# Kernel optimization log

Measured on AMD Instinct MI355X. Metric: run time of the kernel, lower is better.

The kernel has to match this reference:

```python
import jax, jax.numpy as jnp
import numpy as np

NUM_HEADS = 16
PREFIX_LEN = 256


def setup_inputs() -> dict:
    key = jax.random.key(0)
    k1, k2, k3, k4 = jax.random.split(key, 4)
    bs, seq_len, dim = 2, 2048, 1024
    x = jax.random.normal(k1, (bs, seq_len, dim), dtype=jnp.float32)
    # torch Linear weights: (out_features, in_features)
    qkv_w = jax.random.normal(k2, (3 * dim, dim), dtype=jnp.float32) * (dim ** -0.5)
    proj_w = jax.random.normal(k3, (dim, dim), dtype=jnp.float32) * (dim ** -0.5)
    proj_b = jax.random.normal(k4, (dim,), dtype=jnp.float32) * 0.01
    # prefix tokens (visible to everyone): first PREFIX_LEN positions
    prefix_mask = (jnp.arange(seq_len)[None, :] < PREFIX_LEN) & jnp.ones((bs, 1), bool)
    return {"x": x, "qkv_w": qkv_w, "proj_w": proj_w, "proj_b": proj_b,
            "prefix_mask": prefix_mask, "num_patches": 2048}


def reference(x, qkv_w, proj_w, proj_b, prefix_mask, num_patches):
    bs, seq_len, dim = x.shape
    h, hd = NUM_HEADS, dim // NUM_HEADS

    # fused QKV projection (no bias)
    qkv = x @ qkv_w.T                                  # (bs, S, 3*dim)
    q, k, v = jnp.split(qkv, 3, axis=-1)
    q = q.reshape(bs, seq_len, h, hd).transpose(0, 2, 1, 3)  # (bs, h, S, hd)
    k = k.reshape(bs, seq_len, h, hd).transpose(0, 2, 1, 3)
    v = v.reshape(bs, seq_len, h, hd).transpose(0, 2, 1, 3)

    # prefix-causal mask: causal tril OR prefix columns, sliced to (S, S)
    tril = jnp.tril(jnp.ones((num_patches, num_patches), dtype=bool))[:seq_len, :seq_len]
    mask = jnp.logical_or(tril[None, :, :], prefix_mask[:, None, :])  # (bs, S, S)

    scores = jnp.einsum('bhqd,bhkd->bhqk', q, k) / jnp.sqrt(jnp.float32(hd))
    scores = jnp.where(mask[:, None, :, :], scores, -jnp.inf)
    attn = jax.nn.softmax(scores, axis=-1)
    out = jnp.einsum('bhqk,bhkd->bhqd', attn, v)       # (bs, h, S, hd)
    out = out.transpose(0, 2, 1, 3).reshape(bs, seq_len, dim)
    return out @ proj_w.T + proj_b
```

## Files before the change

kernel.cpp:

```cpp
#include <hip/hip_runtime.h>
#include <cstdint>

typedef __attribute__((ext_vector_type(8))) _Float16 half8;
typedef __attribute__((ext_vector_type(4))) _Float16 half4;
typedef __attribute__((ext_vector_type(2))) __fp16 fp16x2;
typedef __attribute__((ext_vector_type(4))) float f32x4;

union H8 { half8 v; unsigned u[4]; };
union H2U { fp16x2 h; unsigned u; };

__device__ __forceinline__ void gld_lds16(const void* g, void* l) {
  __builtin_amdgcn_global_load_lds(
      (const __attribute__((address_space(1))) unsigned int*)g,
      (__attribute__((address_space(3))) unsigned int*)l, 16, 0, 0);
}

__global__ __launch_bounds__(256) void cast3_kernel(
    const float* __restrict__ x, const float* __restrict__ w1,
    const float* __restrict__ w2, _Float16* __restrict__ out) {
  int i = blockIdx.x * 256 + threadIdx.x;
  const float* src;
  int off;
  if (i < 1048576)      { src = x;  off = i; }
  else if (i < 1835008) { src = w1; off = i - 1048576; }
  else                  { src = w2; off = i - 1835008; }
  float4 v = ((const float4*)src)[off];
  half4 h;
  h[0] = (_Float16)v.x; h[1] = (_Float16)v.y;
  h[2] = (_Float16)v.z; h[3] = (_Float16)v.w;
  ((half4*)out)[i] = h;
}

template <int EPI>
__global__ __launch_bounds__(256) void gemm_bt(
    const _Float16* __restrict__ A, const _Float16* __restrict__ B, int K,
    _Float16* __restrict__ Qb, _Float16* __restrict__ Kb, _Float16* __restrict__ VbT,
    float* __restrict__ Out, const float* __restrict__ Bias) {
  __shared__ _Float16 Asm[2][128 * 32];
  __shared__ _Float16 Bsm[2][128 * 32];
  const int tid = threadIdx.x;
  const int wave = tid >> 6, lane = tid & 63;
  const int l16 = lane & 15, lg = lane >> 4;
  const int m0 = blockIdx.y * 128, n0 = blockIdx.x * 128;
  const int wr = wave >> 1, wc = wave & 1;
  f32x4 acc[4][4] = {};

  const int d0 = tid, d1 = tid + 256;
  const int row0 = d0 >> 2, cc0 = (d0 & 3) ^ ((row0 >> 1) & 3);
  const int row1 = d1 >> 2, cc1 = (d1 & 3) ^ ((row1 >> 1) & 3);
  const int sread = ((lg ^ ((l16 >> 1) & 3))) * 16;

  auto STAGE = [&](int buf, int k0) {
    gld_lds16(A + (size_t)(m0 + row0) * K + k0 + cc0 * 8, (char*)Asm[buf] + d0 * 16);
    gld_lds16(A + (size_t)(m0 + row1) * K + k0 + cc1 * 8, (char*)Asm[buf] + d1 * 16);
    gld_lds16(B + (size_t)(n0 + row0) * K + k0 + cc0 * 8, (char*)Bsm[buf] + d0 * 16);
    gld_lds16(B + (size_t)(n0 + row1) * K + k0 + cc1 * 8, (char*)Bsm[buf] + d1 * 16);
  };

  STAGE(0, 0);
  int cur = 0;
  for (int k0 = 0; k0 < K; k0 += 32) {
    __syncthreads();
    if (k0 + 32 < K) STAGE(cur ^ 1, k0 + 32);
    const char* Ac = (const char*)Asm[cur];
    const char* Bc = (const char*)Bsm[cur];
    half8 af[4], bf[4];
#pragma unroll
    for (int f = 0; f < 4; f++) {
      af[f] = *(const half8*)(Ac + (wr * 64 + f * 16 + l16) * 64 + sread);
      bf[f] = *(const half8*)(Bc + (wc * 64 + f * 16 + l16) * 64 + sread);
    }
#pragma unroll
    for (int i = 0; i < 4; i++)
#pragma unroll
      for (int j = 0; j < 4; j++)
        acc[i][j] = __builtin_amdgcn_mfma_f32_16x16x32_f16(af[i], bf[j], acc[i][j], 0, 0, 0);
    cur ^= 1;
  }

  if (EPI == 0) {
#pragma unroll
    for (int i = 0; i < 4; i++) {
      int mbase = m0 + wr * 64 + i * 16 + lg * 4;
      int b = mbase >> 11, s = mbase & 2047;
#pragma unroll
      for (int j = 0; j < 4; j++) {
        int n = n0 + wc * 64 + j * 16 + l16;
        int part = n >> 10, f = n & 1023;
        int h = f >> 6, d = f & 63;
        if (part == 2) {
          int x = s & 31;
          int sp = (s & ~31) | (((x >> 2) & 3) << 3) | (((x >> 4) & 1) << 2);
          half4 v;
          v[0] = (_Float16)acc[i][j][0]; v[1] = (_Float16)acc[i][j][1];
          v[2] = (_Float16)acc[i][j][2]; v[3] = (_Float16)acc[i][j][3];
          *(half4*)(VbT + (((size_t)b * 16 + h) * 64 + d) * 2048 + sp) = v;
        } else {
          _Float16* dst = (part == 0) ? Qb : Kb;
          float scale = (part == 0) ? 0.18033688f : 1.0f;
#pragma unroll
          for (int r = 0; r < 4; r++)
            dst[(((size_t)b * 16 + h) * 2048 + (s + r)) * 64 + d] =
                (_Float16)(acc[i][j][r] * scale);
        }
      }
    }
  } else {
#pragma unroll
    for (int i = 0; i < 4; i++) {
      int mbase = m0 + wr * 64 + i * 16 + lg * 4;
#pragma unroll
      for (int j = 0; j < 4; j++) {
        int n = n0 + wc * 64 + j * 16 + l16;
        float bias = Bias[n];
#pragma unroll
        for (int r = 0; r < 4; r++) {
          int m = mbase + r;
          Out[(size_t)m * 1024 + n] = acc[i][j][r] + bias;
        }
      }
    }
  }
}

__global__ __launch_bounds__(256) void attn_kernel(
    const _Float16* __restrict__ Qb, const _Float16* __restrict__ Kb,
    const _Float16* __restrict__ VbT, _Float16* __restrict__ AO) {
  __shared__ _Float16 Ks[2][64 * 64];
  __shared__ _Float16 Vt[2][64 * 64];
  const int bh = blockIdx.x;
  const int q0 = (31 - blockIdx.y) * 64;
  const int tid = threadIdx.x, wave = tid >> 6, lane = tid & 63;
  const int l16 = lane & 15, lg = lane >> 4;
  const int qw = q0 + wave * 16;
  const size_t bhbase = (size_t)bh * 2048 * 64;
  const _Float16* Kbb = Kb + bhbase;
  const _Float16* Vbb = VbT + bhbase;

  const int c0 = tid, c1 = tid + 256;
  const int kofs0 = ((c0 >> 3) * 64) + (((c0 & 7) ^ ((c0 >> 3) & 7)) * 8);
  const int kofs1 = ((c1 >> 3) * 64) + (((c1 & 7) ^ ((c1 >> 3) & 7)) * 8);
  const int vofs0 = ((c0 >> 3) * 2048) + (((c0 & 7) ^ ((c0 >> 3) & 7)) * 8);
  const int vofs1 = ((c1 >> 3) * 2048) + (((c1 & 7) ^ ((c1 >> 3) & 7)) * 8);

  half8 qf[2];
#pragma unroll
  for (int kc = 0; kc < 2; kc++)
    qf[kc] = *(const half8*)(Qb + bhbase + (size_t)(qw + l16) * 64 + kc * 32 + lg * 8);

  f32x4 oacc[4] = {};
  float lrun = 0.f;
  const int kend = (q0 + 64 > 256) ? (q0 + 64) : 256;

  const int xv = (l16 & 7) << 4;
  const int rb0 = l16 * 128 + ((lg * 16) ^ xv);
  const int rb1 = l16 * 128 + ((64 + lg * 16) ^ xv);

  auto STAGE = [&](int buf, int j0) {
    gld_lds16(Kbb + j0 * 64 + kofs0, (char*)Ks[buf] + c0 * 16);
    gld_lds16(Kbb + j0 * 64 + kofs1, (char*)Ks[buf] + c1 * 16);
    gld_lds16(Vbb + j0 + vofs0, (char*)Vt[buf] + c0 * 16);
    gld_lds16(Vbb + j0 + vofs1, (char*)Vt[buf] + c1 * 16);
  };

  STAGE(0, 0);
  int cur = 0;
  for (int j0 = 0; j0 < kend; j0 += 64) {
    __syncthreads();
    if (j0 + 64 < kend) STAGE(cur ^ 1, j0 + 64);
    const char* Kc = (const char*)Ks[cur];
    const char* Vc = (const char*)Vt[cur];

    f32x4 sf[4] = {};
    __builtin_amdgcn_s_setprio(1);
#pragma unroll
    for (int kc = 0; kc < 2; kc++) {
      const int rb = kc ? rb1 : rb0;
#pragma unroll
      for (int jb = 0; jb < 4; jb++) {
        half8 kf = *(const half8*)(Kc + jb * 2048 + rb);
        sf[jb] = __builtin_amdgcn_mfma_f32_16x16x32_f16(kf, qf[kc], sf[jb], 0, 0, 0);
      }
    }
    __builtin_amdgcn_s_setprio(0);

    if (j0 + 63 >= 256 && j0 + 63 > qw) {
      const int stok = qw + l16;
#pragma unroll
      for (int jb = 0; jb < 4; jb++)
#pragma unroll
        for (int r = 0; r < 4; r++) {
          int j = j0 + jb * 16 + lg * 4 + r;
          if (j > stok && j >= 256) sf[jb][r] = -1e30f;
        }
    }

    float p[16];
#pragma unroll
    for (int jb = 0; jb < 4; jb++)
#pragma unroll
      for (int r = 0; r < 4; r++)
        p[jb * 4 + r] = exp2f(sf[jb][r]);

    float s0 = (p[0] + p[1]) + (p[2] + p[3]);
    float s1 = (p[4] + p[5]) + (p[6] + p[7]);
    float s2 = (p[8] + p[9]) + (p[10] + p[11]);
    float s3 = (p[12] + p[13]) + (p[14] + p[15]);
    lrun += (s0 + s1) + (s2 + s3);

    H8 pf[2];
#pragma unroll
    for (int kc = 0; kc < 2; kc++) {
      H2U t0, t1, t2, t3;
      t0.h = __builtin_amdgcn_cvt_pkrtz(p[kc * 8 + 0], p[kc * 8 + 1]);
      t1.h = __builtin_amdgcn_cvt_pkrtz(p[kc * 8 + 2], p[kc * 8 + 3]);
      t2.h = __builtin_amdgcn_cvt_pkrtz(p[kc * 8 + 4], p[kc * 8 + 5]);
      t3.h = __builtin_amdgcn_cvt_pkrtz(p[kc * 8 + 6], p[kc * 8 + 7]);
      pf[kc].u[0] = t0.u; pf[kc].u[1] = t1.u;
      pf[kc].u[2] = t2.u; pf[kc].u[3] = t3.u;
    }

    __builtin_amdgcn_s_setprio(1);
#pragma unroll
    for (int kc = 0; kc < 2; kc++) {
      const int rb = kc ? rb1 : rb0;
#pragma unroll
      for (int db = 0; db < 4; db++) {
        half8 vf = *(const half8*)(Vc + db * 2048 + rb);
        oacc[db] = __builtin_amdgcn_mfma_f32_16x16x32_f16(vf, pf[kc].v, oacc[db], 0, 0, 0);
      }
    }
    __builtin_amdgcn_s_setprio(0);
    cur ^= 1;
  }

  lrun += __shfl_xor(lrun, 16);
  lrun += __shfl_xor(lrun, 32);

  const int b = bh >> 4, h = bh & 15;
  float inv = 1.0f / lrun;
  int q = qw + l16;
#pragma unroll
  for (int db = 0; db < 4; db++) {
    half4 o;
    o[0] = (_Float16)(oacc[db][0] * inv);
    o[1] = (_Float16)(oacc[db][1] * inv);
    o[2] = (_Float16)(oacc[db][2] * inv);
    o[3] = (_Float16)(oacc[db][3] * inv);
    *(half4*)(AO + ((size_t)b * 2048 + q) * 1024 + h * 64 + db * 16 + lg * 4) = o;
  }
}

extern "C" void kernel_launch(void* const* d_in, const int* in_sizes, int n_in,
                              void* d_out, int out_size, void* d_ws, size_t ws_size,
                              hipStream_t stream) {
  const float* x      = (const float*)d_in[0];
  const float* qkv_w  = (const float*)d_in[1];
  const float* proj_w = (const float*)d_in[2];
  const float* proj_b = (const float*)d_in[3];
  float* out = (float*)d_out;

  char* ws = (char*)d_ws;
  _Float16* Xh  = (_Float16*)(ws);
  _Float16* Wq  = (_Float16*)(ws + ((size_t)8 << 20));
  _Float16* Wp  = (_Float16*)(ws + ((size_t)14 << 20));
  _Float16* Qb  = (_Float16*)(ws + ((size_t)16 << 20));
  _Float16* Kb  = (_Float16*)(ws + ((size_t)24 << 20));
  _Float16* VbT = (_Float16*)(ws + ((size_t)32 << 20));
  _Float16* AO  = (_Float16*)(ws + ((size_t)40 << 20));

  cast3_kernel<<<8192, 256, 0, stream>>>(x, qkv_w, proj_w, Xh);

  gemm_bt<0><<<dim3(24, 32), 256, 0, stream>>>(Xh, Wq, 1024, Qb, Kb, VbT, nullptr, nullptr);
  attn_kernel<<<dim3(32, 32), 256, 0, stream>>>(Qb, Kb, VbT, AO);
  gemm_bt<1><<<dim3(8, 32), 256, 0, stream>>>(AO, Wp, 1024, nullptr, nullptr, nullptr, out, proj_b);
}
```

Baseline: 182.1 us.

## Halve attention query tile and load V fragments directly from global memory

The attention kernel now uses 32-query blocks with 2 waves (128 threads) instead of 64-query blocks with 4 waves, doubling the grid to 32x64. This gives finer causal load balance and more blocks for occupancy. V is no longer staged through LDS; each wave reads its V^T fragments straight from global memory into registers, which halves LDS use. The cost is that K tiles are reused by fewer waves, and the uncached V reads raise global/L2 traffic and latency that is no longer double-buffered.

```diff
diff --git a/kernel.cpp b/kernel.cpp
--- a/kernel.cpp
+++ b/kernel.cpp
@@ -123,44 +123,46 @@
   }
 }
 
-__global__ __launch_bounds__(256) void attn_kernel(
+__global__ __launch_bounds__(128) void attn_kernel(
     const _Float16* __restrict__ Qb, const _Float16* __restrict__ Kb,
     const _Float16* __restrict__ VbT, _Float16* __restrict__ AO) {
   __shared__ _Float16 Ks[2][64 * 64];
-  __shared__ _Float16 Vt[2][64 * 64];
   const int bh = blockIdx.x;
-  const int q0 = (31 - blockIdx.y) * 64;
+  const int q0 = (63 - blockIdx.y) * 32;
   const int tid = threadIdx.x, wave = tid >> 6, lane = tid & 63;
   const int l16 = lane & 15, lg = lane >> 4;
   const int qw = q0 + wave * 16;
   const size_t bhbase = (size_t)bh * 2048 * 64;
   const _Float16* Kbb = Kb + bhbase;
-  const _Float16* Vbb = VbT + bhbase;
-
-  const int c0 = tid, c1 = tid + 256;
-  const int kofs0 = ((c0 >> 3) * 64) + (((c0 & 7) ^ ((c0 >> 3) & 7)) * 8);
-  const int kofs1 = ((c1 >> 3) * 64) + (((c1 & 7) ^ ((c1 >> 3) & 7)) * 8);
-  const int vofs0 = ((c0 >> 3) * 2048) + (((c0 & 7) ^ ((c0 >> 3) & 7)) * 8);
-  const int vofs1 = ((c1 >> 3) * 2048) + (((c1 & 7) ^ ((c1 >> 3) & 7)) * 8);
+
+  int kofs[4], cdst[4];
+#pragma unroll
+  for (int i = 0; i < 4; i++) {
+    int c = tid + i * 128;
+    cdst[i] = c;
+    kofs[i] = ((c >> 3) * 64) + (((c & 7) ^ ((c >> 3) & 7)) * 8);
+  }
 
   half8 qf[2];
 #pragma unroll
   for (int kc = 0; kc < 2; kc++)
     qf[kc] = *(const half8*)(Qb + bhbase + (size_t)(qw + l16) * 64 + kc * 32 + lg * 8);
 
+  const _Float16* Vl = VbT + bhbase + (size_t)l16 * 2048 + lg * 8;
+
   f32x4 oacc[4] = {};
   float lrun = 0.f;
-  const int kend = (q0 + 64 > 256) ? (q0 + 64) : 256;
+  int kend = (q0 + 32 + 63) & ~63;
+  if (kend < 256) kend = 256;
 
   const int xv = (l16 & 7) << 4;
   const int rb0 = l16 * 128 + ((lg * 16) ^ xv);
   const int rb1 = l16 * 128 + ((64 + lg * 16) ^ xv);
 
   auto STAGE = [&](int buf, int j0) {
-    gld_lds16(Kbb + j0 * 64 + kofs0, (char*)Ks[buf] + c0 * 16);
-    gld_lds16(Kbb + j0 * 64 + kofs1, (char*)Ks[buf] + c1 * 16);
-    gld_lds16(Vbb + j0 + vofs0, (char*)Vt[buf] + c0 * 16);
-    gld_lds16(Vbb + j0 + vofs1, (char*)Vt[buf] + c1 * 16);
+#pragma unroll
+    for (int i = 0; i < 4; i++)
+      gld_lds16(Kbb + j0 * 64 + kofs[i], (char*)Ks[buf] + cdst[i] * 16);
   };
 
   STAGE(0, 0);
@@ -169,7 +171,6 @@
     __syncthreads();
     if (j0 + 64 < kend) STAGE(cur ^ 1, j0 + 64);
     const char* Kc = (const char*)Ks[cur];
-    const char* Vc = (const char*)Vt[cur];
 
     f32x4 sf[4] = {};
     __builtin_amdgcn_s_setprio(1);
@@ -183,6 +184,13 @@
       }
     }
     __builtin_amdgcn_s_setprio(0);
+
+    half8 vf[2][4];
+#pragma unroll
+    for (int kc = 0; kc < 2; kc++)
+#pragma unroll
+      for (int db = 0; db < 4; db++)
+        vf[kc][db] = *(const half8*)(Vl + (size_t)(db * 16) * 2048 + j0 + kc * 32);
 
     if (j0 + 63 >= 256 && j0 + 63 > qw) {
       const int stok = qw + l16;
@@ -222,14 +230,10 @@
 
     __builtin_amdgcn_s_setprio(1);
 #pragma unroll
-    for (int kc = 0; kc < 2; kc++) {
-      const int rb = kc ? rb1 : rb0;
-#pragma unroll
-      for (int db = 0; db < 4; db++) {
-        half8 vf = *(const half8*)(Vc + db * 2048 + rb);
-        oacc[db] = __builtin_amdgcn_mfma_f32_16x16x32_f16(vf, pf[kc].v, oacc[db], 0, 0, 0);
-      }
-    }
+    for (int kc = 0; kc < 2; kc++)
+#pragma unroll
+      for (int db = 0; db < 4; db++)
+        oacc[db] = __builtin_amdgcn_mfma_f32_16x16x32_f16(vf[kc][db], pf[kc].v, oacc[db], 0, 0, 0);
     __builtin_amdgcn_s_setprio(0);
     cur ^= 1;
   }
@@ -272,6 +276,6 @@
   cast3_kernel<<<8192, 256, 0, stream>>>(x, qkv_w, proj_w, Xh);
 
   gemm_bt<0><<<dim3(24, 32), 256, 0, stream>>>(Xh, Wq, 1024, Qb, Kb, VbT, nullptr, nullptr);
-  attn_kernel<<<dim3(32, 32), 256, 0, stream>>>(Qb, Kb, VbT, AO);
+  attn_kernel<<<dim3(32, 64), 128, 0, stream>>>(Qb, Kb, VbT, AO);
   gemm_bt<1><<<dim3(8, 32), 256, 0, stream>>>(AO, Wp, 1024, nullptr, nullptr, nullptr, out, proj_b);
 }
```

Measured after the change: 218.2 us. 1.2x slower.
